# Kernel optimization log

Hardware: AMD Instinct MI355X
Metric: run time of the kernel (lower is better)

## Reference

```python
import jax, jax.numpy as jnp
import numpy as np

N_OBJS = 100          # max detections / scatter buffer size
TOP_K = 100           # top_k_n peaks per channel
KP_THRES = 0.3        # score threshold before NMS
NMS_IOU = 0.5
RESIZE_H, RESIZE_W = 1536.0, 1536.0   # resize_shape (== heatmap HxW here)
H, W = 1536, 1536


def _peak_hms(hms):
    # 3x3 stride-1 SAME max pool; keep only local maxima (Base.apply_max_pool)
    hmax = jax.lax.reduce_window(hms, -jnp.inf, jax.lax.max, (1, 3, 3, 1), (1, 1, 1, 1), 'SAME')
    return jnp.where(hms == hmax, hms, 0.0)


def _top_k_loc(hms, k):
    # per-channel top-k peak coordinates -> [b, c, k, 2] (y, x) int32
    b, h, w, c = hms.shape
    flat = jnp.transpose(hms, (0, 3, 1, 2)).reshape(b, c, h * w)
    _, idx = jax.lax.top_k(flat, k)
    return jnp.stack([idx // w, idx % w], axis=-1).astype(jnp.int32)


def _iou_matrix(boxes):
    # boxes [N,4] = (y1,x1,y2,x2)
    y1, x1, y2, x2 = boxes[:, 0], boxes[:, 1], boxes[:, 2], boxes[:, 3]
    area = jnp.maximum(y2 - y1, 0.0) * jnp.maximum(x2 - x1, 0.0)
    iy1 = jnp.maximum(y1[:, None], y1[None, :]); ix1 = jnp.maximum(x1[:, None], x1[None, :])
    iy2 = jnp.minimum(y2[:, None], y2[None, :]); ix2 = jnp.minimum(x2[:, None], x2[None, :])
    inter = jnp.maximum(iy2 - iy1, 0.0) * jnp.maximum(ix2 - ix1, 0.0)
    union = area[:, None] + area[None, :] - inter
    return inter / jnp.maximum(union, 1e-8)


def _nms_single(boxes, scores):
    # greedy single-class NMS, fixed-size (combined_non_max_suppression equivalent,
    # clip_boxes=False, score_threshold=-inf); padded slots are zeros like TF.
    order = jnp.argsort(-scores)
    boxes, scores = boxes[order], scores[order]
    n = boxes.shape[0]
    iou = _iou_matrix(boxes)
    idxs = jnp.arange(n)

    def step(suppressed, inp):
        i, iou_row = inp
        keep_i = ~suppressed[i]
        return suppressed | (keep_i & (iou_row > NMS_IOU) & (idxs > i)), keep_i

    _, keep = jax.lax.scan(step, jnp.zeros(n, bool), (idxs, iou))
    perm = jnp.argsort(jnp.where(keep, 0, 1))  # stable: compact kept to front, score order preserved
    keep_s = keep[perm]
    out_boxes = jnp.where(keep_s[:, None], boxes[perm], 0.0)
    out_scores = jnp.where(keep_s, scores[perm], 0.0)
    return out_boxes, out_scores, jnp.zeros(n, jnp.float32)


def _forward(obj_heat_map, offset_map, size_maps, origin_shapes):
    resize_shape = jnp.array([RESIZE_H, RESIZE_W], jnp.float32)
    ratio = origin_shapes / resize_shape                      # [b,2]
    hms = _peak_hms(obj_heat_map)                             # [b,H,W,2]
    b = hms.shape[0]
    coors = _top_k_loc(hms, TOP_K)                            # [b,2,K,2]
    b_coors, b_lnmks = coors[:, :1], coors[:, 1:]             # obj / nose coords
    bidx = jnp.arange(b)[:, None, None]

    # nose landmark: scores at nose-channel peaks, masked mean of coords (int mean like TF)
    nose_scores = hms[bidx, b_lnmks[..., 0], b_lnmks[..., 1], 1]     # [b,1,K]
    nose_mask = nose_scores > 0.5
    cnt = jnp.maximum(jnp.sum(nose_mask), 1)
    lnmk_mean = jnp.sum(jnp.where(nose_mask[..., None], b_lnmks, 0), axis=(0, 1, 2)) // cnt
    b_lnmks_m = lnmk_mean.reshape(b, 1, 2)                    # requires b == 1 (as in original)
    b_nose_scores = jnp.where(nose_mask, nose_scores, -1.0).reshape(b, -1)

    # boxes from sizes at object peaks
    size_vals = size_maps[bidx, b_coors[..., 0], b_coors[..., 1]]    # [b,1,K,2]
    obj_scores = hms[bidx, b_coors[..., 0], b_coors[..., 1], 0]      # [b,1,K]
    centers = b_coors.astype(jnp.float32)
    tls = jnp.maximum(centers - size_vals / 2.0, 0.0)
    brs = jnp.minimum(centers + size_vals / 2.0, resize_shape - 1.0)
    bboxes = jnp.concatenate([tls, brs], axis=-1) * jnp.tile(ratio, (1, 2))[:, None, None, :]
    bboxes, scores = bboxes[:, 0], obj_scores[:, 0]           # [b,K,4], [b,K]

    # scatter masked candidates into -1-initialized buffer (tensor_scatter_nd_update equivalent)
    mask = scores > KP_THRES
    cand = jnp.where(mask[..., None], jnp.concatenate([bboxes, scores[..., None]], -1), -1.0)
    cand = jnp.pad(cand, ((0, 0), (0, N_OBJS - TOP_K), (0, 0)), constant_values=-1.0)  # [b,N_OBJS,5]

    nb, ns, nc = jax.vmap(_nms_single)(cand[..., :4], cand[..., 4])
    box_results = jnp.where(nb == -1.0, jnp.inf, nb)
    box_results = jnp.where(box_results == 0.0, jnp.inf, box_results)  # (x - 1 == -1)
    b_bboxes = jnp.concatenate([box_results, ns[..., None], nc[..., None]], axis=-1)  # [b,N_OBJS,6]

    # offset vectors at the mean nose landmark (gather 8ch -> [b,n,4,2])
    bidx2 = jnp.arange(b)[:, None]
    off = offset_map[bidx2, b_lnmks_m[..., 0], b_lnmks_m[..., 1]].reshape(b, 1, 4, 2)
    lf = b_lnmks_m.astype(jnp.float32)
    b_ENM = (lf[:, :, None, :] - off) * ratio[:, None, None, :]
    b_lnmks_out = lf * ratio[:, None, :]
    return b_bboxes, b_lnmks_out, b_ENM, b_nose_scores


def setup_inputs() -> dict:
    key = jax.random.key(0)
    k1, k2, k3 = jax.random.split(key, 3)
    obj_heat_map = jax.random.uniform(k1, (1, H, W, 2), jnp.float32)
    offset_map = jax.random.normal(k2, (1, H, W, 8), jnp.float32) * 8.0
    size_maps = jax.random.uniform(k3, (1, H, W, 2), jnp.float32) * 128.0
    origin_shapes = jnp.array([[1080.0, 1920.0]], jnp.float32)
    return {"obj_heat_map": obj_heat_map, "offset_map": offset_map,
            "size_maps": size_maps, "origin_shapes": origin_shapes}


def reference(obj_heat_map, offset_map, size_maps, origin_shapes):
    return _forward(obj_heat_map, offset_map, size_maps, origin_shapes)
```

## Files before the change

### kernel.cpp

```cpp
#include <hip/hip_runtime.h>
#include <cstdint>

#define IW 1536
#define IH 1536
#define TOPK 100
#define CAPP 327680
#define CAPB 128
#define CAPT 8192
#define BF_INF16 0x7F7Fu

typedef unsigned u32; typedef unsigned long long u64; typedef unsigned short u16;

#define OH1   0
#define OCNT  4096
#define OSEL  4102
#define OLSD  4106
#define OZEND 4172
#define OPK   4172
#define OPV   (OPK + 2*CAPP)
#define OLB   (OPV + CAPP)
#define OLT   (OLB + 4*CAPB)

__device__ __forceinline__ u32 enc16(u32 b){ b &= 0xFFFFu; return (b & 0x8000u) ? ((~b)&0xFFFFu) : (b|0x8000u); }
__device__ __forceinline__ u32 dec16(u32 e){ return (e & 0x8000u) ? (e^0x8000u) : ((~e)&0xFFFFu); }
__device__ __forceinline__ float up16(u32 b){ return __uint_as_float((b&0xFFFFu)<<16); }
__device__ __forceinline__ u16 f2bf(float f){ u32 u=__float_as_uint(f); return (u16)((u + 0x7FFFu + ((u>>16)&1u))>>16); }

__device__ __forceinline__ void wave_sel2048(const u32* bins, u32 need, int* Dout, u32* Aout){
  int lane = threadIdx.x & 63;
  u32 s = 0;
  #pragma unroll
  for(int k=0;k<32;++k) s += bins[lane*32+k];
  u32 c = s;
  #pragma unroll
  for(int off=1;off<64;off<<=1){
    u32 v = __shfl_down(c, off, 64);
    if(lane + off < 64) c += v;
  }
  u32 cnext = __shfl_down(c, 1, 64); if(lane==63) cnext = 0u;
  u64 m = __ballot(c >= need);
  if(m == 0ull){ if(lane==0){ *Dout = 0; *Aout = 0u; } return; }
  int L = 63 - __builtin_clzll((unsigned long long)m);
  if(lane == L){
    u32 above = cnext; int D = 32*L;
    for(int b=32*L+31; b>=32*L; --b){
      u32 h = bins[b];
      if(above + h >= need){ D = b; break; }
      above += h;
    }
    *Dout = D; *Aout = above;
  }
}

__global__ __launch_bounds__(1024) void scan_kernel(const u32* __restrict__ hm, u32* __restrict__ ws){
  __shared__ u32 lh[4096];
  __shared__ u32 lbuf[2][1600];
  __shared__ u16 vbuf[2][1600];
  __shared__ u32 lcnt[2], lbase[2];
  int tid = threadIdx.x, lane = tid & 63;
  for(int i=tid;i<4096;i+=1024) lh[i]=0u;
  if(tid<2) lcnt[tid]=0u;
  __syncthreads();

  int p = (blockIdx.x*1024 + tid)*4;
  int y = p / IW, x = p - y*IW;
  const u32* R1 = hm + y*IW;
  const u32* R0 = y ? R1 - IW : R1;
  const u32* R2 = (y < IH-1) ? R1 + IW : R1;
  uint4 c0 = *(const uint4*)(R0+x), c1 = *(const uint4*)(R1+x), c2 = *(const uint4*)(R2+x);
  int xl = x ? x-1 : 0, xr = (x+4 < IW) ? x+4 : IW-1;
  u32 a0[6] = {R0[xl], c0.x, c0.y, c0.z, c0.w, R0[xr]};
  u32 a1[6] = {R1[xl], c1.x, c1.y, c1.z, c1.w, R1[xr]};
  u32 a2[6] = {R2[xl], c2.x, c2.y, c2.z, c2.w, R2[xr]};

  #pragma unroll
  for(int j=0;j<4;++j){
    u32 cc = a1[j+1];
    u32 cl = cc & 0xFFFFu, chv = cc >> 16;
    u32 m0=0u, m1=0u;
    #pragma unroll
    for(int d=0;d<3;++d){
      u32 n0=a0[j+d], n2=a2[j+d]; u32 t;
      t=n0&0xFFFFu; m0=t>m0?t:m0;  t=n0>>16; m1=t>m1?t:m1;
      t=n2&0xFFFFu; m0=t>m0?t:m0;  t=n2>>16; m1=t>m1?t:m1;
    }
    { u32 n=a1[j];   u32 t=n&0xFFFFu; m0=t>m0?t:m0; t=n>>16; m1=t>m1?t:m1; }
    { u32 n=a1[j+2]; u32 t=n&0xFFFFu; m0=t>m0?t:m0; t=n>>16; m1=t>m1?t:m1; }
    bool pk0 = (cl >= m0), pk1 = (chv >= m1);
    u32 idx = (u32)(p + j);

    u64 mk0 = __ballot(pk0);
    if(mk0){
      u32 cw = __popcll(mk0), b;
      if(lane==0) b = atomicAdd(&lcnt[0], cw);
      b = __shfl(b, 0);
      if(pk0){
        u32 pos = b + __popcll(mk0 & ((1ull<<lane)-1ull));
        if(pos < 1600){ lbuf[0][pos] = idx; vbuf[0][pos] = (u16)cl; }
      }
    }
    u64 mk1 = __ballot(pk1);
    if(mk1){
      u32 cw = __popcll(mk1), b;
      if(lane==0) b = atomicAdd(&lcnt[1], cw);
      b = __shfl(b, 0);
      if(pk1){
        u32 pos = b + __popcll(mk1 & ((1ull<<lane)-1ull));
        if(pos < 1600){ lbuf[1][pos] = idx; vbuf[1][pos] = (u16)chv; }
      }
    }
    if(pk0) atomicAdd(&lh[enc16(cl)>>5], 1u);
    if(pk1) atomicAdd(&lh[2048 + (enc16(chv)>>5)], 1u);
  }
  __syncthreads();
  if(tid < 2){
    u32 n = lcnt[tid]; if(n > 1600) n = 1600;
    lcnt[tid] = n;
    lbase[tid] = atomicAdd(&ws[OCNT+tid], n);
  }
  __syncthreads();
  u16* pv = (u16*)(ws + OPV);
  for(int ch=0;ch<2;++ch){
    u32 n = lcnt[ch], base = lbase[ch];
    for(u32 i=tid;i<n;i+=1024){
      u32 g = base + i;
      if(g < CAPP){ ws[OPK + ch*CAPP + g] = lbuf[ch][i]; pv[ch*CAPP + g] = vbuf[ch][i]; }
    }
  }
  for(int i=tid;i<4096;i+=1024) if(lh[i]) atomicAdd(&ws[OH1+i], lh[i]);
}

#define GRID2 128
__global__ __launch_bounds__(1024) void mid_kernel(u32* __restrict__ ws){
  __shared__ u32 lhh[4096];
  __shared__ u64 tbuf[2][2048];
  __shared__ u32 tcnt[2], tbase[2];
  __shared__ u32 lsdl[64];
  __shared__ int Dsh[2]; __shared__ u32 Ash[2];
  int tid = threadIdx.x, lane = tid & 63;
  for(int i=tid;i<4096;i+=1024) lhh[i] = ws[OH1+i];
  if(tid < 2) tcnt[tid] = 0u;
  if(tid < 64) lsdl[tid] = 0u;
  __syncthreads();
  if(tid < 64)       wave_sel2048(lhh,        (u32)TOPK, &Dsh[0], &Ash[0]);
  else if(tid < 128) wave_sel2048(lhh + 2048, (u32)TOPK, &Dsh[1], &Ash[1]);
  __syncthreads();
  if(blockIdx.x == 0 && tid < 2){ ws[OSEL+tid] = (u32)Dsh[tid]; ws[OSEL+2+tid] = Ash[tid]; }

  const u16* pv = (const u16*)(ws + OPV);
  u64* listB = (u64*)(ws + OLB);
  for(int ch=0;ch<2;++ch){
    u32 n = ws[OCNT+ch]; if(n > CAPP) n = CAPP;
    int D = Dsh[ch];
    for(u32 base = blockIdx.x*1024; base < n; base += GRID2*1024){
      u32 i = base + tid;
      bool act = (i < n);
      u32 e = 0, idx = 0;
      if(act){ e = enc16(pv[ch*CAPP + i]); idx = ws[OPK + ch*CAPP + i]; }
      if(act && (int)(e>>5) > D){
        u32 pos = atomicAdd(&ws[OCNT+2+ch], 1u);
        if(pos < CAPB) listB[ch*CAPB + pos] = ((u64)e<<32) | (u32)(~idx);
      }
      bool isT = act && ((int)(e>>5) == D);
      if(isT) atomicAdd(&lsdl[ch*32 + (e & 31u)], 1u);
      u64 mk = __ballot(isT);
      if(mk){
        u32 cw = __popcll(mk), b;
        if(lane==0) b = atomicAdd(&tcnt[ch], cw);
        b = __shfl(b, 0);
        if(isT){
          u32 pos = b + __popcll(mk & ((1ull<<lane)-1ull));
          if(pos < 2048) tbuf[ch][pos] = ((u64)e<<32) | (u32)(~idx);
        }
      }
    }
  }
  __syncthreads();
  if(tid < 2){
    u32 c = tcnt[tid]; if(c > 2048) c = 2048;
    tcnt[tid] = c;
    tbase[tid] = atomicAdd(&ws[OCNT+4+tid], c);
  }
  __syncthreads();
  u64* tie = (u64*)(ws + OLT);
  for(int ch=0;ch<2;++ch)
    for(u32 i=tid;i<tcnt[ch];i+=1024){
      u32 g = tbase[ch] + i;
      if(g < CAPT) tie[ch*CAPT + g] = tbuf[ch][i];
    }
  if(tid < 64 && lsdl[tid]) atomicAdd(&ws[OLSD + tid], lsdl[tid]);
}

__global__ __launch_bounds__(512) void finalize_kernel(
    u32* __restrict__ ws, const u32* __restrict__ szm, const u16* __restrict__ offm,
    const u16* __restrict__ orig, u16* __restrict__ out){
  __shared__ u32 tidxS[2][CAPT];
  __shared__ u32 h2s[2][2048];
  __shared__ u64 keysS[2][CAPB];
  __shared__ u32 selS[2][CAPB];
  __shared__ u32 wbitsS[2][64];
  __shared__ u32 lsdS[64];
  __shared__ u32 hdr[10];
  __shared__ int selcS[2], selc2S[2], BvS[2], LshS[2], tcS[2];
  __shared__ float oval[TOPK]; __shared__ int oidx[TOPK];
  __shared__ float nval[TOPK]; __shared__ int nidx[TOPK];
  __shared__ float cbox[TOPK][4]; __shared__ float cscore[TOPK]; __shared__ float area[TOPK];
  __shared__ int sup[TOPK]; __shared__ int slotv[TOPK];
  __shared__ u64 nbits[2*TOPK];
  __shared__ u64 suppS[2];
  __shared__ int cS, srS, scS, meanr, meanc;
  int tid = threadIdx.x, lane = tid & 63;
  int ch = tid >> 8, ltid = tid & 255;

  if(tid < 10) hdr[tid] = ws[OCNT + tid];
  if(tid < 64) lsdS[tid] = ws[OLSD + tid];
  for(int i=tid;i<4096;i+=512) ((u32*)h2s)[i] = 0u;
  if(tid < 128) ((u32*)wbitsS)[tid] = 0u;
  if(tid < 4){ selcS[tid&1] = 0; selc2S[tid&1] = 0; }
  if(tid < 2){ BvS[tid] = 0; LshS[tid] = 0; tcS[tid] = 0; }
  if(tid < TOPK){ oval[tid]=0.0f; oidx[tid]=0; nval[tid]=0.0f; nidx[tid]=0; }
  __syncthreads();

  int nB = (int)hdr[2+ch]; if(nB > CAPB) nB = CAPB;
  int nT = (int)hdr[4+ch]; if(nT > CAPT) nT = CAPT;
  int D  = (int)hdr[6+ch];
  u32 above = hdr[8+ch];
  const u64* listB = ((const u64*)(ws + OLB)) + ch*CAPB;
  const u64* tie   = ((const u64*)(ws + OLT)) + ch*CAPT;
  float* dval = ch ? nval : oval;
  int*   didx = ch ? nidx : oidx;

  if(ltid < 64){
    u32 h = (lane < 32) ? lsdS[ch*32 + lane] : 0u;
    u32 c = h;
    #pragma unroll
    for(int off=1;off<32;off<<=1){
      u32 v = __shfl_down(c, off, 64);
      if(lane + off < 32) c += v;
    }
    u32 need2 = (u32)TOPK - above;
    u64 m = __ballot(lane >= 1 && lane < 32 && c >= need2);
    if(lane == 0){
      LshS[ch] = m ? (63 - __builtin_clzll((unsigned long long)m)) : 0;
      selcS[ch] = nB;
    }
  }
  for(int i=ltid;i<nB;i+=256) keysS[ch][i] = listB[i];
  __syncthreads();
  u32 thr = ((u32)D<<5) | (u32)LshS[ch];
  float tval = up16(dec16(thr));

  for(int base2=0; base2<nT; base2+=256){
    int i = base2 + ltid;
    bool act = (i < nT);
    u64 k = 0; u32 e = 0, idx = 0;
    if(act){ k = tie[i]; e = (u32)(k>>32); idx = ~(u32)(k & 0xFFFFFFFFu); }
    if(act && e > thr){
      int pos = atomicAdd(&selcS[ch], 1); if(pos < CAPB) keysS[ch][pos] = k;
    }
    bool isT = act && (e == thr);
    u64 mk = __ballot(isT);
    if(mk){
      u32 cw = __popcll(mk), b;
      if(lane==0) b = (u32)atomicAdd(&tcS[ch], (int)cw);
      b = __shfl(b, 0);
      if(isT){
        u32 pos = b + __popcll(mk & ((1ull<<lane)-1ull));
        if(pos < CAPT) tidxS[ch][pos] = idx;
      }
    }
    if(isT) atomicAdd(&h2s[ch][idx>>11], 1u);
  }
  __syncthreads();

  int nA = selcS[ch]; if(nA > CAPB) nA = CAPB; if(nA > TOPK) nA = TOPK;
  int need = TOPK - nA;
  if(ltid < nA){
    u64 kreg = keysS[ch][ltid];
    int r = 0;
    for(int j=0;j<nA;++j) r += (keysS[ch][j] > kreg);
    if(r < TOPK){
      dval[r] = up16(dec16((u32)(kreg>>32)));
      didx[r] = (int)(~(u32)(kreg & 0xFFFFFFFFu));
    }
  }
  if(ltid < 64){
    const u32* hh = h2s[ch];
    int base = lane*32;
    u32 s = 0;
    #pragma unroll
    for(int k2=0;k2<32;++k2) s += hh[base+k2];
    u32 c = s;
    #pragma unroll
    for(int off=1;off<64;off<<=1){
      u32 v = __shfl_up(c, off, 64);
      if(lane >= off) c += v;
    }
    u64 m = __ballot(need > 0 && c >= (u32)need);
    int L = m ? (int)(__ffsll((unsigned long long)m) - 1) : -1;
    if(L >= 0 && lane == L){
      u32 hb[32];
      #pragma unroll
      for(int k2=0;k2<32;++k2) hb[k2] = hh[base+k2];
      u32 cum2 = c - s;
      int Bsel = base;
      #pragma unroll
      for(int k2=0;k2<32;++k2){
        if(cum2 + hb[k2] >= (u32)need){ Bsel = base+k2; break; }
        cum2 += hb[k2];
      }
      BvS[ch] = Bsel;
    }
  }
  __syncthreads();

  int B = BvS[ch];
  int tc = tcS[ch]; if(tc > CAPT) tc = CAPT;
  if(need > 0){
    for(int i=ltid;i<tc;i+=256){
      u32 idx = tidxS[ch][i];
      int b = (int)(idx>>11);
      if(b < B){
        int pos = atomicAdd(&selc2S[ch], 1);
        if(pos < CAPB) selS[ch][pos] = idx;
      } else if(b == B){
        atomicOr(&wbitsS[ch][(idx&2047)>>5], 1u<<(idx&31));
      }
    }
  }
  __syncthreads();

  int sc = selc2S[ch]; if(sc > CAPB) sc = CAPB;
  if(need > 0 && ltid < sc){
    u32 v = selS[ch][ltid];
    int r = 0;
    for(int j=0;j<sc;++j) r += (selS[ch][j] < v);
    if(nA + r < TOPK){ dval[nA+r] = tval; didx[nA+r] = (int)v; }
  }
  if(need > 0 && ltid < 64){
    u32 bits = wbitsS[ch][ltid];
    u32 cnt = __popc(bits);
    u32 incl = cnt;
    #pragma unroll
    for(int off=1;off<64;off<<=1){
      u32 v = __shfl_up(incl, off, 64);
      if(lane >= off) incl += v;
    }
    int excl = (int)(incl - cnt);
    int rem = need - sc;
    int pos = nA + sc + excl;
    int j = 0;
    while(bits){
      int l = __ffs(bits) - 1; bits &= bits - 1;
      if(excl + j < rem && pos + j < TOPK){
        dval[pos+j] = tval;
        didx[pos+j] = (int)(((u32)B<<11) | ((u32)ltid<<5) | (u32)l);
      }
      ++j;
    }
  }
  __syncthreads();

  float ry = up16(orig[0]) / 1536.0f;
  float rx = up16(orig[1]) / 1536.0f;

  if(tid == 0){ cS = 0; srS = 0; scS = 0; }
  __syncthreads();
  if(tid < TOPK && nval[tid] > 0.5f){
    atomicAdd(&cS, 1);
    atomicAdd(&srS, nidx[tid] / IW);
    atomicAdd(&scS, nidx[tid] % IW);
  }
  if(tid < TOPK) out[610 + tid] = f2bf(nval[tid] > 0.5f ? nval[tid] : -1.0f);
  __syncthreads();
  if(tid == 0){
    int c = cS < 1 ? 1 : cS;
    meanr = srS / c; meanc = scS / c;
  }

  if(tid < TOPK){
    int idx = oidx[tid];
    int r = idx / IW, c = idx - r*IW;
    float score = oval[tid];
    u32 sz = szm[idx];
    float sy = up16(sz), sx = up16(sz>>16);
    float cy = (float)r, cx = (float)c;
    float tly = fmaxf(cy - sy*0.5f, 0.0f);
    float tlx = fmaxf(cx - sx*0.5f, 0.0f);
    float bry = fminf(cy + sy*0.5f, 1535.0f);
    float brx = fminf(cx + sx*0.5f, 1535.0f);
    bool mk = score > 0.3f;
    float b0 = mk ? tly*ry : -1.0f;
    float b1 = mk ? tlx*rx : -1.0f;
    float b2 = mk ? bry*ry : -1.0f;
    float b3 = mk ? brx*rx : -1.0f;
    cbox[tid][0]=b0; cbox[tid][1]=b1; cbox[tid][2]=b2; cbox[tid][3]=b3;
    cscore[tid] = mk ? score : -1.0f;
    area[tid] = fmaxf(b2-b0,0.0f) * fmaxf(b3-b1,0.0f);
  }
  if(tid < 2*TOPK) nbits[tid] = 0ull;
  __syncthreads();

  for(int t=tid; t<TOPK*TOPK; t+=512){
    int i = t / TOPK, j = t - i*TOPK;
    if(j > i){
      float iy1 = fmaxf(cbox[i][0], cbox[j][0]);
      float ix1 = fmaxf(cbox[i][1], cbox[j][1]);
      float iy2 = fminf(cbox[i][2], cbox[j][2]);
      float ix2 = fminf(cbox[i][3], cbox[j][3]);
      float inter = fmaxf(iy2-iy1,0.0f) * fmaxf(ix2-ix1,0.0f);
      float uni = (area[i] + area[j]) - inter;
      if(inter / fmaxf(uni, 1e-8f) > 0.5f)
        atomicOr(&nbits[i*2 + (j>>6)], 1ull << (j&63));
    }
  }
  __syncthreads();
  if(tid == 0){
    u64 s0 = 0ull, s1 = 0ull;
    for(int base=0;base<TOPK;base+=10){
      u64 buf[20];
      #pragma unroll
      for(int k=0;k<20;++k) buf[k] = nbits[2*base+k];
      #pragma unroll
      for(int k=0;k<10;++k){
        int i = base+k;
        bool su = (i<64) ? ((s0>>i)&1ull) : ((s1>>(i-64))&1ull);
        if(!su){ s0 |= buf[2*k]; s1 |= buf[2*k+1]; }
      }
    }
    suppS[0] = s0; suppS[1] = s1;
  }
  __syncthreads();
  if(tid < TOPK) sup[tid] = (int)((suppS[tid>>6] >> (tid&63)) & 1ull);
  __syncthreads();

  if(tid < TOPK){
    int kbefore = 0, sbefore = 0, ktot = 0;
    for(int j=0;j<TOPK;++j){
      int sj = sup[j];
      ktot += (1 - sj);
      if(j < tid){ kbefore += (1 - sj); sbefore += sj; }
    }
    int slot = sup[tid] ? (ktot + sbefore) : kbefore;
    slotv[slot] = tid;
  }
  __syncthreads();

  if(tid < TOPK){
    int s = slotv[tid];
    bool ks = !sup[s];
    u16 row[6];
    if(ks){
      for(int d=0;d<4;++d){
        float v = cbox[s][d];
        row[d] = (v == -1.0f || v == 0.0f) ? (u16)BF_INF16 : f2bf(v);
      }
      row[4] = f2bf(cscore[s]);
    } else {
      for(int d=0;d<4;++d) row[d] = (u16)BF_INF16;
      row[4] = 0;
    }
    row[5] = 0;
    for(int d=0;d<6;++d) out[tid*6 + d] = row[d];
  }

  if(tid == 0){
    float lfy = (float)meanr, lfx = (float)meanc;
    out[600] = f2bf(lfy * ry);
    out[601] = f2bf(lfx * rx);
    const u16* op = offm + ((size_t)meanr*IW + meanc)*8;
    for(int p=0;p<4;++p){
      out[602 + p*2 + 0] = f2bf((lfy - up16(op[p*2+0])) * ry);
      out[602 + p*2 + 1] = f2bf((lfx - up16(op[p*2+1])) * rx);
    }
  }
}

extern "C" void kernel_launch(void* const* d_in, const int* in_sizes, int n_in,
                              void* d_out, int out_size, void* d_ws, size_t ws_size,
                              hipStream_t stream) {
  const u32* heat = (const u32*)d_in[0];
  const u16* offm = (const u16*)d_in[1];
  const u32* szm  = (const u32*)d_in[2];
  const u16* orig = (const u16*)d_in[3];
  u16* out = (u16*)d_out;
  u32* ws = (u32*)d_ws;

  hipMemsetAsync(ws, 0, OZEND*sizeof(u32), stream);
  scan_kernel<<<576, 1024, 0, stream>>>(heat, ws);
  mid_kernel<<<GRID2, 1024, 0, stream>>>(ws);
  finalize_kernel<<<1, 512, 0, stream>>>(ws, szm, offm, orig, out);
}
```

Measured before the change: 182.8 us.

## Fuse mid and finalize kernels using last-block-done atomic counter

```diff
diff --git a/kernel.cpp b/kernel.cpp
--- a/kernel.cpp
+++ b/kernel.cpp
@@ -15,6 +15,7 @@
 #define OCNT  4096
 #define OSEL  4102
 #define OLSD  4106
+#define ODONE 4170
 #define OZEND 4172
 #define OPK   4172
 #define OPV   (OPK + 2*CAPP)
@@ -131,107 +132,127 @@
 }
 
 #define GRID2 128
-__global__ __launch_bounds__(1024) void mid_kernel(u32* __restrict__ ws){
-  __shared__ u32 lhh[4096];
-  __shared__ u64 tbuf[2][2048];
-  __shared__ u32 tcnt[2], tbase[2];
-  __shared__ u32 lsdl[64];
-  __shared__ int Dsh[2]; __shared__ u32 Ash[2];
-  int tid = threadIdx.x, lane = tid & 63;
-  for(int i=tid;i<4096;i+=1024) lhh[i] = ws[OH1+i];
-  if(tid < 2) tcnt[tid] = 0u;
-  if(tid < 64) lsdl[tid] = 0u;
-  __syncthreads();
-  if(tid < 64)       wave_sel2048(lhh,        (u32)TOPK, &Dsh[0], &Ash[0]);
-  else if(tid < 128) wave_sel2048(lhh + 2048, (u32)TOPK, &Dsh[1], &Ash[1]);
-  __syncthreads();
-  if(blockIdx.x == 0 && tid < 2){ ws[OSEL+tid] = (u32)Dsh[tid]; ws[OSEL+2+tid] = Ash[tid]; }
-
-  const u16* pv = (const u16*)(ws + OPV);
-  u64* listB = (u64*)(ws + OLB);
-  for(int ch=0;ch<2;++ch){
-    u32 n = ws[OCNT+ch]; if(n > CAPP) n = CAPP;
-    int D = Dsh[ch];
-    for(u32 base = blockIdx.x*1024; base < n; base += GRID2*1024){
-      u32 i = base + tid;
-      bool act = (i < n);
-      u32 e = 0, idx = 0;
-      if(act){ e = enc16(pv[ch*CAPP + i]); idx = ws[OPK + ch*CAPP + i]; }
-      if(act && (int)(e>>5) > D){
-        u32 pos = atomicAdd(&ws[OCNT+2+ch], 1u);
-        if(pos < CAPB) listB[ch*CAPB + pos] = ((u64)e<<32) | (u32)(~idx);
-      }
-      bool isT = act && ((int)(e>>5) == D);
-      if(isT) atomicAdd(&lsdl[ch*32 + (e & 31u)], 1u);
-      u64 mk = __ballot(isT);
-      if(mk){
-        u32 cw = __popcll(mk), b;
-        if(lane==0) b = atomicAdd(&tcnt[ch], cw);
-        b = __shfl(b, 0);
-        if(isT){
-          u32 pos = b + __popcll(mk & ((1ull<<lane)-1ull));
-          if(pos < 2048) tbuf[ch][pos] = ((u64)e<<32) | (u32)(~idx);
-        }
-      }
-    }
-  }
-  __syncthreads();
-  if(tid < 2){
-    u32 c = tcnt[tid]; if(c > 2048) c = 2048;
-    tcnt[tid] = c;
-    tbase[tid] = atomicAdd(&ws[OCNT+4+tid], c);
-  }
-  __syncthreads();
-  u64* tie = (u64*)(ws + OLT);
-  for(int ch=0;ch<2;++ch)
-    for(u32 i=tid;i<tcnt[ch];i+=1024){
-      u32 g = tbase[ch] + i;
-      if(g < CAPT) tie[ch*CAPT + g] = tbuf[ch][i];
-    }
-  if(tid < 64 && lsdl[tid]) atomicAdd(&ws[OLSD + tid], lsdl[tid]);
-}
-
-__global__ __launch_bounds__(512) void finalize_kernel(
+
+union MFMem {
+  struct {
+    u32 lhh[4096];
+    u64 tbuf[2][2048];
+    u32 tcnt[2], tbase[2];
+    u32 lsdl[64];
+    int Dsh[2]; u32 Ash[2];
+  } m;
+  struct {
+    u32 tidxS[2][CAPT];
+    u32 h2s[2][2048];
+    u64 keysS[2][CAPB];
+    u32 selS[2][CAPB];
+    u32 wbitsS[2][64];
+    u32 lsdS[64];
+    u32 hdr[10];
+    int selcS[2], selc2S[2], BvS[2], LshS[2], tcS[2];
+    float oval[TOPK]; int oidx[TOPK];
+    float nval[TOPK]; int nidx[TOPK];
+    float cbox[TOPK][4]; float cscore[TOPK]; float area[TOPK];
+    int sup[TOPK]; int slotv[TOPK];
+    u64 nbits[2*TOPK];
+    u64 suppS[2];
+    int cS, srS, scS, meanr, meanc;
+  } f;
+};
+
+__global__ __launch_bounds__(512) void midfin_kernel(
     u32* __restrict__ ws, const u32* __restrict__ szm, const u16* __restrict__ offm,
     const u16* __restrict__ orig, u16* __restrict__ out){
-  __shared__ u32 tidxS[2][CAPT];
-  __shared__ u32 h2s[2][2048];
-  __shared__ u64 keysS[2][CAPB];
-  __shared__ u32 selS[2][CAPB];
-  __shared__ u32 wbitsS[2][64];
-  __shared__ u32 lsdS[64];
-  __shared__ u32 hdr[10];
-  __shared__ int selcS[2], selc2S[2], BvS[2], LshS[2], tcS[2];
-  __shared__ float oval[TOPK]; __shared__ int oidx[TOPK];
-  __shared__ float nval[TOPK]; __shared__ int nidx[TOPK];
-  __shared__ float cbox[TOPK][4]; __shared__ float cscore[TOPK]; __shared__ float area[TOPK];
-  __shared__ int sup[TOPK]; __shared__ int slotv[TOPK];
-  __shared__ u64 nbits[2*TOPK];
-  __shared__ u64 suppS[2];
-  __shared__ int cS, srS, scS, meanr, meanc;
+  __shared__ MFMem sm;
+  __shared__ u32 lastFlag;
   int tid = threadIdx.x, lane = tid & 63;
+
+  {
+    for(int i=tid;i<4096;i+=512) sm.m.lhh[i] = ws[OH1+i];
+    if(tid < 2) sm.m.tcnt[tid] = 0u;
+    if(tid < 64) sm.m.lsdl[tid] = 0u;
+    __syncthreads();
+    if(tid < 64)       wave_sel2048(sm.m.lhh,        (u32)TOPK, &sm.m.Dsh[0], &sm.m.Ash[0]);
+    else if(tid < 128) wave_sel2048(sm.m.lhh + 2048, (u32)TOPK, &sm.m.Dsh[1], &sm.m.Ash[1]);
+    __syncthreads();
+    if(blockIdx.x == 0 && tid < 2){ ws[OSEL+tid] = (u32)sm.m.Dsh[tid]; ws[OSEL+2+tid] = sm.m.Ash[tid]; }
+
+    const u16* pv = (const u16*)(ws + OPV);
+    u64* listB = (u64*)(ws + OLB);
+    for(int ch=0;ch<2;++ch){
+      u32 n = ws[OCNT+ch]; if(n > CAPP) n = CAPP;
+      int D = sm.m.Dsh[ch];
+      for(u32 base = blockIdx.x*512; base < n; base += GRID2*512){
+        u32 i = base + tid;
+        bool act = (i < n);
+        u32 e = 0, idx = 0;
+        if(act){ e = enc16(pv[ch*CAPP + i]); idx = ws[OPK + ch*CAPP + i]; }
+        if(act && (int)(e>>5) > D){
+          u32 pos = atomicAdd(&ws[OCNT+2+ch], 1u);
+          if(pos < CAPB) listB[ch*CAPB + pos] = ((u64)e<<32) | (u32)(~idx);
+        }
+        bool isT = act && ((int)(e>>5) == D);
+        if(isT) atomicAdd(&sm.m.lsdl[ch*32 + (e & 31u)], 1u);
+        u64 mk = __ballot(isT);
+        if(mk){
+          u32 cw = __popcll(mk), b;
+          if(lane==0) b = atomicAdd(&sm.m.tcnt[ch], cw);
+          b = __shfl(b, 0);
+          if(isT){
+            u32 pos = b + __popcll(mk & ((1ull<<lane)-1ull));
+            if(pos < 2048) sm.m.tbuf[ch][pos] = ((u64)e<<32) | (u32)(~idx);
+          }
+        }
+      }
+    }
+    __syncthreads();
+    if(tid < 2){
+      u32 c = sm.m.tcnt[tid]; if(c > 2048) c = 2048;
+      sm.m.tcnt[tid] = c;
+      sm.m.tbase[tid] = atomicAdd(&ws[OCNT+4+tid], c);
+    }
+    __syncthreads();
+    u64* tie = (u64*)(ws + OLT);
+    for(int ch=0;ch<2;++ch)
+      for(u32 i=tid;i<sm.m.tcnt[ch];i+=512){
+        u32 g = sm.m.tbase[ch] + i;
+        if(g < CAPT) tie[ch*CAPT + g] = sm.m.tbuf[ch][i];
+      }
+    if(tid < 64 && sm.m.lsdl[tid]) atomicAdd(&ws[OLSD + tid], sm.m.lsdl[tid]);
+  }
+
+  __syncthreads();
+  if(tid == 0){
+    __threadfence();
+    u32 old = __hip_atomic_fetch_add(ws + ODONE, 1u, __ATOMIC_ACQ_REL, __HIP_MEMORY_SCOPE_AGENT);
+    lastFlag = (old == (u32)GRID2 - 1u) ? 1u : 0u;
+  }
+  __syncthreads();
+  if(!lastFlag) return;
+  __threadfence();
+
   int ch = tid >> 8, ltid = tid & 255;
 
-  if(tid < 10) hdr[tid] = ws[OCNT + tid];
-  if(tid < 64) lsdS[tid] = ws[OLSD + tid];
-  for(int i=tid;i<4096;i+=512) ((u32*)h2s)[i] = 0u;
-  if(tid < 128) ((u32*)wbitsS)[tid] = 0u;
-  if(tid < 4){ selcS[tid&1] = 0; selc2S[tid&1] = 0; }
-  if(tid < 2){ BvS[tid] = 0; LshS[tid] = 0; tcS[tid] = 0; }
-  if(tid < TOPK){ oval[tid]=0.0f; oidx[tid]=0; nval[tid]=0.0f; nidx[tid]=0; }
-  __syncthreads();
-
-  int nB = (int)hdr[2+ch]; if(nB > CAPB) nB = CAPB;
-  int nT = (int)hdr[4+ch]; if(nT > CAPT) nT = CAPT;
-  int D  = (int)hdr[6+ch];
-  u32 above = hdr[8+ch];
+  if(tid < 10) sm.f.hdr[tid] = ws[OCNT + tid];
+  if(tid < 64) sm.f.lsdS[tid] = ws[OLSD + tid];
+  for(int i=tid;i<4096;i+=512) ((u32*)sm.f.h2s)[i] = 0u;
+  if(tid < 128) ((u32*)sm.f.wbitsS)[tid] = 0u;
+  if(tid < 4){ sm.f.selcS[tid&1] = 0; sm.f.selc2S[tid&1] = 0; }
+  if(tid < 2){ sm.f.BvS[tid] = 0; sm.f.LshS[tid] = 0; sm.f.tcS[tid] = 0; }
+  if(tid < TOPK){ sm.f.oval[tid]=0.0f; sm.f.oidx[tid]=0; sm.f.nval[tid]=0.0f; sm.f.nidx[tid]=0; }
+  __syncthreads();
+
+  int nB = (int)sm.f.hdr[2+ch]; if(nB > CAPB) nB = CAPB;
+  int nT = (int)sm.f.hdr[4+ch]; if(nT > CAPT) nT = CAPT;
+  int D  = (int)sm.f.hdr[6+ch];
+  u32 above = sm.f.hdr[8+ch];
   const u64* listB = ((const u64*)(ws + OLB)) + ch*CAPB;
   const u64* tie   = ((const u64*)(ws + OLT)) + ch*CAPT;
-  float* dval = ch ? nval : oval;
-  int*   didx = ch ? nidx : oidx;
+  float* dval = ch ? sm.f.nval : sm.f.oval;
+  int*   didx = ch ? sm.f.nidx : sm.f.oidx;
 
   if(ltid < 64){
-    u32 h = (lane < 32) ? lsdS[ch*32 + lane] : 0u;
+    u32 h = (lane < 32) ? sm.f.lsdS[ch*32 + lane] : 0u;
     u32 c = h;
     #pragma unroll
     for(int off=1;off<32;off<<=1){
@@ -241,13 +262,13 @@
     u32 need2 = (u32)TOPK - above;
     u64 m = __ballot(lane >= 1 && lane < 32 && c >= need2);
     if(lane == 0){
-      LshS[ch] = m ? (63 - __builtin_clzll((unsigned long long)m)) : 0;
-      selcS[ch] = nB;
-    }
-  }
-  for(int i=ltid;i<nB;i+=256) keysS[ch][i] = listB[i];
-  __syncthreads();
-  u32 thr = ((u32)D<<5) | (u32)LshS[ch];
+      sm.f.LshS[ch] = m ? (63 - __builtin_clzll((unsigned long long)m)) : 0;
+      sm.f.selcS[ch] = nB;
+    }
+  }
+  for(int i=ltid;i<nB;i+=256) sm.f.keysS[ch][i] = listB[i];
+  __syncthreads();
+  u32 thr = ((u32)D<<5) | (u32)sm.f.LshS[ch];
   float tval = up16(dec16(thr));
 
   for(int base2=0; base2<nT; base2+=256){
@@ -256,36 +277,36 @@
     u64 k = 0; u32 e = 0, idx = 0;
     if(act){ k = tie[i]; e = (u32)(k>>32); idx = ~(u32)(k & 0xFFFFFFFFu); }
     if(act && e > thr){
-      int pos = atomicAdd(&selcS[ch], 1); if(pos < CAPB) keysS[ch][pos] = k;
+      int pos = atomicAdd(&sm.f.selcS[ch], 1); if(pos < CAPB) sm.f.keysS[ch][pos] = k;
     }
     bool isT = act && (e == thr);
     u64 mk = __ballot(isT);
     if(mk){
       u32 cw = __popcll(mk), b;
-      if(lane==0) b = (u32)atomicAdd(&tcS[ch], (int)cw);
+      if(lane==0) b = (u32)atomicAdd(&sm.f.tcS[ch], (int)cw);
       b = __shfl(b, 0);
       if(isT){
         u32 pos = b + __popcll(mk & ((1ull<<lane)-1ull));
-        if(pos < CAPT) tidxS[ch][pos] = idx;
-      }
-    }
-    if(isT) atomicAdd(&h2s[ch][idx>>11], 1u);
-  }
-  __syncthreads();
-
-  int nA = selcS[ch]; if(nA > CAPB) nA = CAPB; if(nA > TOPK) nA = TOPK;
+        if(pos < CAPT) sm.f.tidxS[ch][pos] = idx;
+      }
+    }
+    if(isT) atomicAdd(&sm.f.h2s[ch][idx>>11], 1u);
+  }
+  __syncthreads();
+
+  int nA = sm.f.selcS[ch]; if(nA > CAPB) nA = CAPB; if(nA > TOPK) nA = TOPK;
   int need = TOPK - nA;
   if(ltid < nA){
-    u64 kreg = keysS[ch][ltid];
+    u64 kreg = sm.f.keysS[ch][ltid];
     int r = 0;
-    for(int j=0;j<nA;++j) r += (keysS[ch][j] > kreg);
+    for(int j=0;j<nA;++j) r += (sm.f.keysS[ch][j] > kreg);
     if(r < TOPK){
       dval[r] = up16(dec16((u32)(kreg>>32)));
       didx[r] = (int)(~(u32)(kreg & 0xFFFFFFFFu));
     }
   }
   if(ltid < 64){
-    const u32* hh = h2s[ch];
+    const u32* hh = sm.f.h2s[ch];
     int base = lane*32;
     u32 s = 0;
     #pragma unroll
@@ -309,36 +330,36 @@
         if(cum2 + hb[k2] >= (u32)need){ Bsel = base+k2; break; }
         cum2 += hb[k2];
       }
-      BvS[ch] = Bsel;
-    }
-  }
-  __syncthreads();
-
-  int B = BvS[ch];
-  int tc = tcS[ch]; if(tc > CAPT) tc = CAPT;
+      sm.f.BvS[ch] = Bsel;
+    }
+  }
+  __syncthreads();
+
+  int B = sm.f.BvS[ch];
+  int tc = sm.f.tcS[ch]; if(tc > CAPT) tc = CAPT;
   if(need > 0){
     for(int i=ltid;i<tc;i+=256){
-      u32 idx = tidxS[ch][i];
+      u32 idx = sm.f.tidxS[ch][i];
       int b = (int)(idx>>11);
       if(b < B){
-        int pos = atomicAdd(&selc2S[ch], 1);
-        if(pos < CAPB) selS[ch][pos] = idx;
+        int pos = atomicAdd(&sm.f.selc2S[ch], 1);
+        if(pos < CAPB) sm.f.selS[ch][pos] = idx;
       } else if(b == B){
-        atomicOr(&wbitsS[ch][(idx&2047)>>5], 1u<<(idx&31));
-      }
-    }
-  }
-  __syncthreads();
-
-  int sc = selc2S[ch]; if(sc > CAPB) sc = CAPB;
+        atomicOr(&sm.f.wbitsS[ch][(idx&2047)>>5], 1u<<(idx&31));
+      }
+    }
+  }
+  __syncthreads();
+
+  int sc = sm.f.selc2S[ch]; if(sc > CAPB) sc = CAPB;
   if(need > 0 && ltid < sc){
-    u32 v = selS[ch][ltid];
+    u32 v = sm.f.selS[ch][ltid];
     int r = 0;
-    for(int j=0;j<sc;++j) r += (selS[ch][j] < v);
+    for(int j=0;j<sc;++j) r += (sm.f.selS[ch][j] < v);
     if(nA + r < TOPK){ dval[nA+r] = tval; didx[nA+r] = (int)v; }
   }
   if(need > 0 && ltid < 64){
-    u32 bits = wbitsS[ch][ltid];
+    u32 bits = sm.f.wbitsS[ch][ltid];
     u32 cnt = __popc(bits);
     u32 incl = cnt;
     #pragma unroll
@@ -364,24 +385,24 @@
   float ry = up16(orig[0]) / 1536.0f;
   float rx = up16(orig[1]) / 1536.0f;
 
-  if(tid == 0){ cS = 0; srS = 0; scS = 0; }
-  __syncthreads();
-  if(tid < TOPK && nval[tid] > 0.5f){
-    atomicAdd(&cS, 1);
-    atomicAdd(&srS, nidx[tid] / IW);
-    atomicAdd(&scS, nidx[tid] % IW);
-  }
-  if(tid < TOPK) out[610 + tid] = f2bf(nval[tid] > 0.5f ? nval[tid] : -1.0f);
+  if(tid == 0){ sm.f.cS = 0; sm.f.srS = 0; sm.f.scS = 0; }
+  __syncthreads();
+  if(tid < TOPK && sm.f.nval[tid] > 0.5f){
+    atomicAdd(&sm.f.cS, 1);
+    atomicAdd(&sm.f.srS, sm.f.nidx[tid] / IW);
+    atomicAdd(&sm.f.scS, sm.f.nidx[tid] % IW);
+  }
+  if(tid < TOPK) out[610 + tid] = f2bf(sm.f.nval[tid] > 0.5f ? sm.f.nval[tid] : -1.0f);
   __syncthreads();
   if(tid == 0){
-    int c = cS < 1 ? 1 : cS;
-    meanr = srS / c; meanc = scS / c;
+    int c = sm.f.cS < 1 ? 1 : sm.f.cS;
+    sm.f.meanr = sm.f.srS / c; sm.f.meanc = sm.f.scS / c;
   }
 
   if(tid < TOPK){
-    int idx = oidx[tid];
+    int idx = sm.f.oidx[tid];
     int r = idx / IW, c = idx - r*IW;
-    float score = oval[tid];
+    float score = sm.f.oval[tid];
     u32 sz = szm[idx];
     float sy = up16(sz), sx = up16(sz>>16);
     float cy = (float)r, cx = (float)c;
@@ -394,68 +415,68 @@
     float b1 = mk ? tlx*rx : -1.0f;
     float b2 = mk ? bry*ry : -1.0f;
     float b3 = mk ? brx*rx : -1.0f;
-    cbox[tid][0]=b0; cbox[tid][1]=b1; cbox[tid][2]=b2; cbox[tid][3]=b3;
-    cscore[tid] = mk ? score : -1.0f;
-    area[tid] = fmaxf(b2-b0,0.0f) * fmaxf(b3-b1,0.0f);
-  }
-  if(tid < 2*TOPK) nbits[tid] = 0ull;
+    sm.f.cbox[tid][0]=b0; sm.f.cbox[tid][1]=b1; sm.f.cbox[tid][2]=b2; sm.f.cbox[tid][3]=b3;
+    sm.f.cscore[tid] = mk ? score : -1.0f;
+    sm.f.area[tid] = fmaxf(b2-b0,0.0f) * fmaxf(b3-b1,0.0f);
+  }
+  if(tid < 2*TOPK) sm.f.nbits[tid] = 0ull;
   __syncthreads();
 
   for(int t=tid; t<TOPK*TOPK; t+=512){
     int i = t / TOPK, j = t - i*TOPK;
     if(j > i){
-      float iy1 = fmaxf(cbox[i][0], cbox[j][0]);
-      float ix1 = fmaxf(cbox[i][1], cbox[j][1]);
-      float iy2 = fminf(cbox[i][2], cbox[j][2]);
-      float ix2 = fminf(cbox[i][3], cbox[j][3]);
+      float iy1 = fmaxf(sm.f.cbox[i][0], sm.f.cbox[j][0]);
+      float ix1 = fmaxf(sm.f.cbox[i][1], sm.f.cbox[j][1]);
+      float iy2 = fminf(sm.f.cbox[i][2], sm.f.cbox[j][2]);
+      float ix2 = fminf(sm.f.cbox[i][3], sm.f.cbox[j][3]);
       float inter = fmaxf(iy2-iy1,0.0f) * fmaxf(ix2-ix1,0.0f);
-      float uni = (area[i] + area[j]) - inter;
+      float uni = (sm.f.area[i] + sm.f.area[j]) - inter;
       if(inter / fmaxf(uni, 1e-8f) > 0.5f)
-        atomicOr(&nbits[i*2 + (j>>6)], 1ull << (j&63));
+        atomicOr(&sm.f.nbits[i*2 + (j>>6)], 1ull << (j&63));
     }
   }
   __syncthreads();
   if(tid == 0){
     u64 s0 = 0ull, s1 = 0ull;
-    for(int base=0;base<TOPK;base+=10){
-      u64 buf[20];
+    for(int base=0;base<TOPK;base+=5){
+      u64 buf[10];
       #pragma unroll
-      for(int k=0;k<20;++k) buf[k] = nbits[2*base+k];
+      for(int k=0;k<10;++k) buf[k] = sm.f.nbits[2*base+k];
       #pragma unroll
-      for(int k=0;k<10;++k){
+      for(int k=0;k<5;++k){
         int i = base+k;
         bool su = (i<64) ? ((s0>>i)&1ull) : ((s1>>(i-64))&1ull);
         if(!su){ s0 |= buf[2*k]; s1 |= buf[2*k+1]; }
       }
     }
-    suppS[0] = s0; suppS[1] = s1;
-  }
-  __syncthreads();
-  if(tid < TOPK) sup[tid] = (int)((suppS[tid>>6] >> (tid&63)) & 1ull);
+    sm.f.suppS[0] = s0; sm.f.suppS[1] = s1;
+  }
+  __syncthreads();
+  if(tid < TOPK) sm.f.sup[tid] = (int)((sm.f.suppS[tid>>6] >> (tid&63)) & 1ull);
   __syncthreads();
 
   if(tid < TOPK){
     int kbefore = 0, sbefore = 0, ktot = 0;
     for(int j=0;j<TOPK;++j){
-      int sj = sup[j];
+      int sj = sm.f.sup[j];
       ktot += (1 - sj);
       if(j < tid){ kbefore += (1 - sj); sbefore += sj; }
     }
-    int slot = sup[tid] ? (ktot + sbefore) : kbefore;
-    slotv[slot] = tid;
+    int slot = sm.f.sup[tid] ? (ktot + sbefore) : kbefore;
+    sm.f.slotv[slot] = tid;
   }
   __syncthreads();
 
   if(tid < TOPK){
-    int s = slotv[tid];
-    bool ks = !sup[s];
+    int s = sm.f.slotv[tid];
+    bool ks = !sm.f.sup[s];
     u16 row[6];
     if(ks){
       for(int d=0;d<4;++d){
-        float v = cbox[s][d];
+        float v = sm.f.cbox[s][d];
         row[d] = (v == -1.0f || v == 0.0f) ? (u16)BF_INF16 : f2bf(v);
       }
-      row[4] = f2bf(cscore[s]);
+      row[4] = f2bf(sm.f.cscore[s]);
     } else {
       for(int d=0;d<4;++d) row[d] = (u16)BF_INF16;
       row[4] = 0;
@@ -465,10 +486,10 @@
   }
 
   if(tid == 0){
-    float lfy = (float)meanr, lfx = (float)meanc;
+    float lfy = (float)sm.f.meanr, lfx = (float)sm.f.meanc;
     out[600] = f2bf(lfy * ry);
     out[601] = f2bf(lfx * rx);
-    const u16* op = offm + ((size_t)meanr*IW + meanc)*8;
+    const u16* op = offm + ((size_t)sm.f.meanr*IW + sm.f.meanc)*8;
     for(int p=0;p<4;++p){
       out[602 + p*2 + 0] = f2bf((lfy - up16(op[p*2+0])) * ry);
       out[602 + p*2 + 1] = f2bf((lfx - up16(op[p*2+1])) * rx);
@@ -488,6 +509,5 @@
 
   hipMemsetAsync(ws, 0, OZEND*sizeof(u32), stream);
   scan_kernel<<<576, 1024, 0, stream>>>(heat, ws);
-  mid_kernel<<<GRID2, 1024, 0, stream>>>(ws);
-  finalize_kernel<<<1, 512, 0, stream>>>(ws, szm, offm, orig, out);
+  midfin_kernel<<<GRID2, 512, 0, stream>>>(ws, szm, offm, orig, out);
 }
```

Result: slower. 188.9 us (+3.3%).
